# Optimization experiments

Hardware: AMD Instinct MI355X
Metric: run time of the kernel (lower is better)

Reference implementation:

```python
import jax, jax.numpy as jnp
import numpy as np

N, E = 4096, 131072
IN, HID, OUT = 128, 128, 256
H4, C4 = 4, HID            # first/middle GAT: 4 heads of 128 -> concat 512
CAT = H4 * C4              # 512
NH, DK = 8, OUT // 8       # dense MHA
EPS_LN = 1e-5


def setup_inputs() -> dict:
    key = jax.random.key(0)
    ks = jax.random.split(key, 32)
    s = 0.05
    inp = {
        "x": jax.random.normal(ks[0], (N, IN), jnp.float32),
        "edge_index": jax.random.randint(ks[1], (2, E), 0, N, jnp.int64),
        # GAT layer 0: in=128, heads=4, out=128
        "W0": jax.random.normal(ks[2], (IN, H4 * C4)) * s,
        "as0": jax.random.normal(ks[3], (H4, C4)) * s,
        "ad0": jax.random.normal(ks[4], (H4, C4)) * s,
        "b0": jnp.zeros((H4 * C4,)),
        # GAT layer 1: in=512, heads=4, out=128
        "W1": jax.random.normal(ks[5], (CAT, H4 * C4)) * s,
        "as1": jax.random.normal(ks[6], (H4, C4)) * s,
        "ad1": jax.random.normal(ks[7], (H4, C4)) * s,
        "b1": jnp.zeros((H4 * C4,)),
        # GAT layer 2: in=512, heads=1, out=256
        "W2": jax.random.normal(ks[8], (CAT, OUT)) * s,
        "as2": jax.random.normal(ks[9], (1, OUT)) * s,
        "ad2": jax.random.normal(ks[10], (1, OUT)) * s,
        "b2": jnp.zeros((OUT,)),
        # LayerNorms
        "g0": jnp.ones((CAT,)), "be0": jnp.zeros((CAT,)),
        "g1": jnp.ones((CAT,)), "be1": jnp.zeros((CAT,)),
        "g2": jnp.ones((OUT,)), "be2": jnp.zeros((OUT,)),
        # dense MHA on output_dim=256
        "wq": jax.random.normal(ks[11], (OUT, OUT)) * s, "bq": jnp.zeros((OUT,)),
        "wk": jax.random.normal(ks[12], (OUT, OUT)) * s, "bk": jnp.zeros((OUT,)),
        "wv": jax.random.normal(ks[13], (OUT, OUT)) * s, "bv": jnp.zeros((OUT,)),
        "wo": jax.random.normal(ks[14], (OUT, OUT)) * s, "bo": jnp.zeros((OUT,)),
    }
    return inp


def _layer_norm(x, g, b):
    mu = x.mean(-1, keepdims=True)
    var = ((x - mu) ** 2).mean(-1, keepdims=True)
    return (x - mu) * jax.lax.rsqrt(var + EPS_LN) * g + b


def _gat(x, src, dst, W, a_src, a_dst, bias, heads, out_c):
    # PyG GATConv (concat=True, negative_slope=0.2, self-loops pre-added)
    n = x.shape[0]
    xl = (x @ W).reshape(n, heads, out_c)            # [N,H,C]
    al_s = (xl * a_src).sum(-1)                      # [N,H]
    al_d = (xl * a_dst).sum(-1)                      # [N,H]
    alpha = jax.nn.leaky_relu(al_s[src] + al_d[dst], 0.2)  # [Etot,H]
    m = jax.ops.segment_max(alpha, dst, num_segments=n)
    e = jnp.exp(alpha - m[dst])
    denom = jax.ops.segment_sum(e, dst, num_segments=n)
    w = e / (denom[dst] + 1e-16)                     # [Etot,H]
    msg = w[:, :, None] * xl[src]                    # [Etot,H,C]
    out = jax.ops.segment_sum(msg, dst, num_segments=n)
    return out.reshape(n, heads * out_c) + bias


def _mha(x, wq, bq, wk, bk, wv, bv, wo, bo):
    # x: [1,N,D], 8 heads
    B, S, D = x.shape
    def split(y):
        return y.reshape(B, S, NH, DK).transpose(0, 2, 1, 3)
    Q, K, V = split(x @ wq + bq), split(x @ wk + bk), split(x @ wv + bv)
    scores = jnp.einsum('bhqd,bhkd->bhqk', Q, K) / np.sqrt(DK)
    attn = jax.nn.softmax(scores, axis=-1)
    out = jnp.einsum('bhqk,bhkd->bhqd', attn, V)
    out = out.transpose(0, 2, 1, 3).reshape(B, S, D)
    return out @ wo + bo


def reference(x, edge_index, W0, as0, ad0, b0, W1, as1, ad1, b1, W2, as2, ad2, b2,
              g0, be0, g1, be1, g2, be2, wq, bq, wk, bk, wv, bv, wo, bo):
    n = x.shape[0]
    loops = jnp.arange(n, dtype=edge_index.dtype)
    src = jnp.concatenate([edge_index[0], loops])
    dst = jnp.concatenate([edge_index[1], loops])

    # layer 0: in=128 -> 512; residual None (128 != 512)
    h = jax.nn.elu(_gat(x, src, dst, W0, as0, ad0, b0, H4, C4))
    h = _layer_norm(h, g0, be0)

    # layer 1: 512 -> 512; residual applies
    res = h
    h = jax.nn.elu(_gat(h, src, dst, W1, as1, ad1, b1, H4, C4))
    h = _layer_norm(h, g1, be1)
    h = h + res

    # layer 2: 512 -> 256, 1 head
    h = _gat(h, src, dst, W2, as2, ad2, b2, 1, OUT)
    h = _layer_norm(h, g2, be2)

    # dense self-attention over all nodes as one sequence
    h = _mha(h[None], wq, bq, wk, bk, wv, bv, wo, bo)[0]
    return h
```

## Files before the change

kernel.cpp:

```cpp
#include <hip/hip_runtime.h>
#include <math.h>

typedef __attribute__((ext_vector_type(8))) short short8;
typedef __attribute__((ext_vector_type(4))) float float4v;

#define QS 0.17677669529663687f

__device__ __forceinline__ float waveReduceSum(float v){
  #pragma unroll
  for(int o=32;o>0;o>>=1) v += __shfl_down(v,o,64);
  return v;
}

__device__ __forceinline__ unsigned short f2bf(float f){
  unsigned int u = __float_as_uint(f);
  return (unsigned short)((u + 0x7FFFu + ((u>>16)&1u)) >> 16);
}
__device__ __forceinline__ float bf2f(unsigned short u){
  return __uint_as_float(((unsigned int)u)<<16);
}

__global__ __launch_bounds__(256) void prep(const float* __restrict__ x, unsigned short* __restrict__ xb,
                     const float* __restrict__ W0, unsigned short* __restrict__ W0t,
                     const float* __restrict__ W1, unsigned short* __restrict__ W1t,
                     const float* __restrict__ W2, unsigned short* __restrict__ W2t,
                     const float* __restrict__ wq, const float* __restrict__ wk,
                     const float* __restrict__ wv, unsigned short* __restrict__ wqkvt,
                     const float* __restrict__ bq, const float* __restrict__ bk,
                     const float* __restrict__ bv, float* __restrict__ bqkv,
                     const float* __restrict__ wo, unsigned short* __restrict__ wot,
                     const float* __restrict__ as0, const float* __restrict__ ad0, unsigned short* __restrict__ S0,
                     const float* __restrict__ as1, const float* __restrict__ ad1, unsigned short* __restrict__ S1,
                     const float* __restrict__ as2, const float* __restrict__ ad2, unsigned short* __restrict__ S2){
  int b = blockIdx.x, t = threadIdx.x;
  if(b < 2048){ int i = b*256 + t; xb[i] = f2bf(x[i]); return; }
  if(b == 4864){ bqkv[t] = bq[t]*QS; bqkv[256+t] = bk[t]; bqkv[512+t] = bv[t]; return; }
  if(b >= 4865){
    int bb = b - 4865;
    const float *W,*as,*ad; unsigned short* S; int K,C,H,k;
    if(bb<128){W=W0;as=as0;ad=ad0;S=S0;K=128;C=128;H=4;k=bb;}
    else if(bb<640){W=W1;as=as1;ad=ad1;S=S1;K=512;C=128;H=4;k=bb-128;}
    else {W=W2;as=as2;ad=ad2;S=S2;K=512;C=256;H=1;k=bb-640;}
    int D = H*C;
    __shared__ float s1[4], s2[4];
    int lane=t&63, wid=t>>6;
    for(int h=0;h<H;h++){
      float ps=0.f, pd=0.f;
      for(int c=t;c<C;c+=256){
        float wv2 = W[k*D + h*C + c];
        ps += wv2*as[h*C+c];
        pd += wv2*ad[h*C+c];
      }
      ps = waveReduceSum(ps); pd = waveReduceSum(pd);
      if(lane==0){ s1[wid]=ps; s2[wid]=pd; }
      __syncthreads();
      if(t==0){
        float u=s1[0]+s1[1]+s1[2]+s1[3], v=s2[0]+s2[1]+s2[2]+s2[3];
        S[h*K+k]=f2bf(u); S[(4+h)*K+k]=f2bf(v);
      }
      __syncthreads();
    }
    if(t==0){
      for(int h=H;h<4;h++){ S[h*K+k]=0; S[(4+h)*K+k]=0; }
      for(int r=8;r<16;r++) S[r*K+k]=0;
    }
    return;
  }
  const float* src; unsigned short* dst; int K,N,base,roff; float sc = 1.f;
  if(b<2304){src=W0;dst=W0t;K=128;N=512;base=2048;roff=0;}
  else if(b<3328){src=W1;dst=W1t;K=512;N=512;base=2304;roff=0;}
  else if(b<3840){src=W2;dst=W2t;K=512;N=256;base=3328;roff=0;}
  else if(b<4096){src=wq;dst=wqkvt;K=256;N=256;base=3840;roff=0;sc=QS;}
  else if(b<4352){src=wk;dst=wqkvt;K=256;N=256;base=4096;roff=256;}
  else if(b<4608){src=wv;dst=wqkvt;K=256;N=256;base=4352;roff=512;}
  else            {src=wo;dst=wot;K=256;N=256;base=4608;roff=0;}
  int idx = (b-base)*256 + t;
  int k = idx / N, n = idx - k*N;
  dst[(n+roff)*K + k] = f2bf(src[idx]*sc);
}

__global__ __launch_bounds__(256) void gemm_mfma(const unsigned short* __restrict__ A,
                                                 const unsigned short* __restrict__ Bt,
                                                 const float* __restrict__ bias,
                                                 float* __restrict__ C,
                                                 unsigned short* __restrict__ Cb,
                                                 const unsigned short* __restrict__ Wsd,
                                                 float* __restrict__ als,
                                                 float* __restrict__ ald,
                                                 int M, int K, int N){
  int t = threadIdx.x, lane = t & 63, w = t >> 6;
  int m = lane & 15, g = lane >> 4;
  int bm = blockIdx.y * 64, bn = blockIdx.x * 64;

  __shared__ unsigned short As[64*72];
  __shared__ unsigned short Bs[64*72];

  int sr = t >> 3;
  int sc = (t & 7) * 8;
  const unsigned short* Ap = A  + (bm + sr)*K + sc;
  const unsigned short* Bp = Bt + (bn + sr)*K + sc;
  bool doC = (Wsd != nullptr) && (blockIdx.x == 0);

  float4v acc[4];
  #pragma unroll
  for(int nt=0;nt<4;nt++) acc[nt] = (float4v){0.f,0.f,0.f,0.f};
  float4v acc2 = (float4v){0.f,0.f,0.f,0.f};

  for(int k0=0;k0<K;k0+=64){
    short8 a0 = *(const short8*)(Ap + k0);
    short8 a1 = *(const short8*)(Ap + 32*K + k0);
    short8 b0 = *(const short8*)(Bp + k0);
    short8 b1 = *(const short8*)(Bp + 32*K + k0);
    __syncthreads();
    *(short8*)&As[sr*72 + sc]      = a0;
    *(short8*)&As[(sr+32)*72 + sc] = a1;
    *(short8*)&Bs[sr*72 + sc]      = b0;
    *(short8*)&Bs[(sr+32)*72 + sc] = b1;
    __syncthreads();

    #pragma unroll
    for(int ks=0;ks<2;ks++){
      short8 aA = *(const short8*)&As[(w*16 + m)*72 + ks*32 + g*8];
      #pragma unroll
      for(int nt=0;nt<4;nt++){
        short8 bB = *(const short8*)&Bs[(nt*16 + m)*72 + ks*32 + g*8];
        acc[nt] = __builtin_amdgcn_mfma_f32_16x16x32_bf16(aA, bB, acc[nt], 0,0,0);
      }
      if(doC){
        short8 bW = *(const short8*)(Wsd + m*K + k0 + ks*32 + g*8);
        acc2 = __builtin_amdgcn_mfma_f32_16x16x32_bf16(aA, bW, acc2, 0,0,0);
      }
    }
  }
  #pragma unroll
  for(int nt=0;nt<4;nt++){
    int col = bn + nt*16 + m;
    float bv = bias ? bias[col] : 0.f;
    #pragma unroll
    for(int r=0;r<4;r++){
      int row = bm + w*16 + g*4 + r;
      float v = acc[nt][r] + bv;
      if(C)  C[row*N + col]  = v;
      if(Cb) Cb[row*N + col] = f2bf(v);
    }
  }
  if(doC){
    #pragma unroll
    for(int r=0;r<4;r++){
      int row = bm + w*16 + g*4 + r;
      if(m<4)      als[row*4 + m]     = acc2[r];
      else if(m<8) ald[row*4 + (m-4)] = acc2[r];
    }
  }
}

__global__ void csr_count(const int* __restrict__ ei, int E, int Etot,
                          int* __restrict__ hist){
  int e = blockIdx.x*256 + threadIdx.x;
  if(e>=Etot) return;
  int d = (e<E) ? (ei[E+e]&4095) : (e-E);
  atomicAdd(&hist[d], 1);
}

__global__ __launch_bounds__(1024) void csr_scan(const int* __restrict__ hist,
                                                 int* __restrict__ row_ptr,
                                                 int* __restrict__ wcnt, int N){
  __shared__ int sh[1024];
  int t = threadIdx.x;
  int base[4];
  int s = 0;
  #pragma unroll
  for(int i=0;i<4;i++){ base[i]=s; s += hist[t*4+i]; }
  sh[t] = s;
  __syncthreads();
  for(int off=1; off<1024; off<<=1){
    int x = (t>=off) ? sh[t-off] : 0;
    __syncthreads();
    sh[t] += x;
    __syncthreads();
  }
  int excl = (t==0) ? 0 : sh[t-1];
  #pragma unroll
  for(int i=0;i<4;i++){
    row_ptr[t*4+i] = excl + base[i];
    wcnt[t*4+i]    = excl + base[i];
  }
  if(t==1023) row_ptr[N] = excl + s;
}

__global__ void csr_scatter(const int* __restrict__ ei, int E, int Etot,
                            int* __restrict__ wcnt, int* __restrict__ col){
  int e = blockIdx.x*256 + threadIdx.x;
  if(e>=Etot) return;
  int s,d;
  if(e<E){ s=ei[e]&4095; d=ei[E+e]&4095; } else { s=d=e-E; }
  int pos = atomicAdd(&wcnt[d], 1);
  col[pos] = s;
}

#define CE 128
__global__ void gat_gather_ln(const int* __restrict__ rp,
                              const int* __restrict__ col,
                              const unsigned short* __restrict__ xlb,
                              const float* __restrict__ als,
                              const float* __restrict__ ald,
                              const float* __restrict__ bias,
                              const float* __restrict__ gw,
                              const float* __restrict__ be,
                              const float* __restrict__ res,
                              float* __restrict__ out,
                              unsigned short* __restrict__ outb,
                              int D, int logC, int do_elu){
  int n = blockIdx.x, t = threadIdx.x;
  int c0 = t*2;
  int h = c0 >> logC;
  int rowW = D >> 1;
  float4 advv = *(const float4*)(ald + n*4);
  int start = rp[n], end = rp[n+1];
  const unsigned int* xw = (const unsigned int*)xlb;

  __shared__ float pw[CE*4];
  __shared__ int offs[CE];

  float acc0=0.f, acc1=0.f, den=0.f;

  for(int base=start; base<end; base+=CE){
    int cnt = min(CE, end-base);
    __syncthreads();
    if(t < cnt){
      int s = col[base+t];
      offs[t] = s*rowW;
      float4 av = *(const float4*)(als + s*4);
      #pragma unroll
      for(int hh=0;hh<4;hh++){
        float a = ((const float*)&av)[hh] + ((const float*)&advv)[hh];
        a = a>0.f ? a : 0.2f*a;
        pw[t*4+hh] = __expf(a);
      }
    }
    __syncthreads();
    #pragma unroll 4
    for(int j=0;j<cnt;j++){
      float p = pw[j*4+h];
      unsigned int u = xw[offs[j] + t];
      acc0 += p * bf2f((unsigned short)(u & 0xffffu));
      acc1 += p * bf2f((unsigned short)(u >> 16));
      den += p;
    }
  }

  float inv_d = 1.f/(den + 1e-16f);
  float v0 = acc0*inv_d + bias[c0];
  float v1 = acc1*inv_d + bias[c0+1];
  if(do_elu){
    v0 = v0>0.f ? v0 : expm1f(v0);
    v1 = v1>0.f ? v1 : expm1f(v1);
  }
  __shared__ float sh[4];
  int lane=t&63, wid=t>>6, nw = blockDim.x>>6;
  float sum = waveReduceSum(v0+v1);
  if(lane==0) sh[wid]=sum;
  __syncthreads();
  float mean = 0.f;
  for(int i=0;i<nw;i++) mean += sh[i];
  mean /= (float)D;
  __syncthreads();
  float d0 = v0-mean, d1 = v1-mean;
  float vs = waveReduceSum(d0*d0 + d1*d1);
  if(lane==0) sh[wid]=vs;
  __syncthreads();
  float var = 0.f;
  for(int i=0;i<nw;i++) var += sh[i];
  var /= (float)D;
  float inv = rsqrtf(var + 1e-5f);
  float y0 = d0*inv*gw[c0]   + be[c0];
  float y1 = d1*inv*gw[c0+1] + be[c0+1];
  if(res){ float2 rv = *(const float2*)(res + n*D + c0); y0 += rv.x; y1 += rv.y; }
  if(out) *(float2*)(out + n*D + c0) = make_float2(y0, y1);
  if(outb) ((unsigned int*)outb)[n*rowW + t] =
      (unsigned int)f2bf(y0) | ((unsigned int)f2bf(y1) << 16);
}

__global__ __launch_bounds__(256) void transpose_v(const unsigned short* __restrict__ QKV,
                                                   unsigned short* __restrict__ Vt, int S){
  __shared__ unsigned short tile[64][72];
  int bs = blockIdx.x*64;
  int bd = blockIdx.y*64;
  int t = threadIdx.x;
  int r8 = t>>3, c8 = (t&7)*8;
  #pragma unroll
  for(int it=0; it<2; it++){
    int row = r8 + it*32;
    short8 v = *(const short8*)(QKV + (bs+row)*768 + 512 + bd + c8);
    *(short8*)&tile[row][c8] = v;
  }
  __syncthreads();
  #pragma unroll
  for(int it=0; it<2; it++){
    int drow = r8 + it*32;
    short8 o;
    #pragma unroll
    for(int j=0;j<8;j++) o[j] = (short)tile[c8+j][drow];
    *(short8*)(Vt + (bd+drow)*S + bs + c8) = o;
  }
}

#define KS 4
__global__ __launch_bounds__(256) void attention10(const unsigned short* __restrict__ QKV,
                                                   const unsigned short* __restrict__ Vt,
                                                   float* __restrict__ Op,
                                                   float* __restrict__ lp, int S){
  const int RS = 768;
  int qb = blockIdx.x * 64;
  int h  = blockIdx.y;
  int ks = blockIdx.z;
  int t  = threadIdx.x;
  int lane = t & 63, w = t >> 6;
  int m = lane & 15, g = lane >> 4;

  __shared__ unsigned short Ps[64*72];
  __shared__ unsigned short Vs[32*72];
  __shared__ unsigned short Ks[64*36];

  short8 aQ = *(const short8*)(QKV + (qb + w*16 + m)*RS + h*32 + g*8);

  float4v o0 = {0.f,0.f,0.f,0.f}, o1 = {0.f,0.f,0.f,0.f};
  float l = 0.f;

  int r8 = t>>3, c8 = (t&7)*8;
  int kr = t>>2, kc = (t&3)*8;
  int kA = ks*(S/KS), kB = kA + S/KS;

  for(int kt=kA; kt<kB; kt+=64){
    short8 v = *(const short8*)(Vt + (h*32 + r8)*S + kt + c8);
    short8 kv = *(const short8*)(QKV + (kt + kr)*RS + 256 + h*32 + kc);
    __syncthreads();
    *(short8*)&Vs[r8*72 + c8] = v;
    *(short8*)&Ks[kr*36 + kc] = kv;
    __syncthreads();

    #pragma unroll
    for(int nt=0;nt<4;nt++){
      short8 aK = *(const short8*)&Ks[(nt*16 + m)*36 + g*8];
      float4v acc = {0.f,0.f,0.f,0.f};
      acc = __builtin_amdgcn_mfma_f32_16x16x32_bf16(aK, aQ, acc, 0,0,0);
      float p0 = __expf(acc[0]);
      float p1 = __expf(acc[1]);
      float p2 = __expf(acc[2]);
      float p3 = __expf(acc[3]);
      l += (p0+p1) + (p2+p3);
      unsigned int r0 = __float_as_uint(p0) + 0x8000u;
      unsigned int r1 = __float_as_uint(p1) + 0x8000u;
      unsigned int r2 = __float_as_uint(p2) + 0x8000u;
      unsigned int r3 = __float_as_uint(p3) + 0x8000u;
      uint2 pk;
      pk.x = __builtin_amdgcn_perm(r1, r0, 0x07060302u);
      pk.y = __builtin_amdgcn_perm(r3, r2, 0x07060302u);
      *(uint2*)&Ps[(w*16 + m)*72 + nt*16 + g*4] = pk;
    }

    #pragma unroll
    for(int kh=0;kh<2;kh++){
      short8 aP  = *(const short8*)&Ps[(w*16 + m)*72 + kh*32 + g*8];
      short8 bV0 = *(const short8*)&Vs[(m)*72    + kh*32 + g*8];
      short8 bV1 = *(const short8*)&Vs[(16+m)*72 + kh*32 + g*8];
      o0 = __builtin_amdgcn_mfma_f32_16x16x32_bf16(aP, bV0, o0, 0,0,0);
      o1 = __builtin_amdgcn_mfma_f32_16x16x32_bf16(aP, bV1, o1, 0,0,0);
    }
  }

  l += __shfl_xor(l, 16, 64);
  l += __shfl_xor(l, 32, 64);

  float* Ob = Op + (size_t)ks*S*256;
  #pragma unroll
  for(int r=0;r<4;r++){
    int q = qb + w*16 + g*4 + r;
    Ob[q*256 + h*32 + m]      = o0[r];
    Ob[q*256 + h*32 + 16 + m] = o1[r];
  }
  if(g==0) lp[ks*S*8 + (qb + w*16 + m)*8 + h] = l;
}

__global__ __launch_bounds__(256) void combine(const float* __restrict__ Op,
                                               const float* __restrict__ lp,
                                               unsigned short* __restrict__ aob, int S){
  int q = blockIdx.x, t = threadIdx.x;
  int h = t >> 5;
  float o = 0.f, l = 0.f;
  #pragma unroll
  for(int s=0;s<KS;s++) o += Op[(size_t)s*S*256 + q*256 + t];
  #pragma unroll
  for(int s=0;s<KS;s++) l += lp[s*S*8 + q*8 + h];
  aob[q*256 + t] = f2bf(o / l);
}

extern "C" void kernel_launch(void* const* d_in, const int* in_sizes, int n_in,
                              void* d_out, int out_size, void* d_ws, size_t ws_size,
                              hipStream_t stream) {
  const float* x   = (const float*)d_in[0];
  const int*   ei  = (const int*)d_in[1];
  const float* W0  = (const float*)d_in[2];
  const float* as0 = (const float*)d_in[3];
  const float* ad0 = (const float*)d_in[4];
  const float* b0  = (const float*)d_in[5];
  const float* W1  = (const float*)d_in[6];
  const float* as1 = (const float*)d_in[7];
  const float* ad1 = (const float*)d_in[8];
  const float* b1  = (const float*)d_in[9];
  const float* W2  = (const float*)d_in[10];
  const float* as2 = (const float*)d_in[11];
  const float* ad2 = (const float*)d_in[12];
  const float* b2  = (const float*)d_in[13];
  const float* g0  = (const float*)d_in[14];
  const float* be0 = (const float*)d_in[15];
  const float* g1  = (const float*)d_in[16];
  const float* be1 = (const float*)d_in[17];
  const float* g2  = (const float*)d_in[18];
  const float* be2 = (const float*)d_in[19];
  const float* wq  = (const float*)d_in[20];
  const float* bq  = (const float*)d_in[21];
  const float* wk  = (const float*)d_in[22];
  const float* bk  = (const float*)d_in[23];
  const float* wv  = (const float*)d_in[24];
  const float* bv  = (const float*)d_in[25];
  const float* wo  = (const float*)d_in[26];
  const float* bo  = (const float*)d_in[27];
  float* out = (float*)d_out;

  const int N = 4096;
  const int E = in_sizes[1] / 2;
  const int Etot = E + N;

  char* p = (char*)d_ws;
  auto alloc = [&](size_t bytes){ char* r = p; p += (bytes + 255) & ~(size_t)255; return r; };

  float* h0   = (float*)alloc(N*512*4);
  float* als  = (float*)alloc(N*4*4);
  float* ald  = (float*)alloc(N*4*4);
  unsigned short* xb   = (unsigned short*)alloc(N*128*2);
  unsigned short* xlb  = (unsigned short*)alloc(N*512*2);
  unsigned short* h0b  = (unsigned short*)alloc(N*512*2);
  unsigned short* h1b  = (unsigned short*)alloc(N*512*2);
  unsigned short* h2b  = (unsigned short*)alloc(N*256*2);
  unsigned short* QKVb = (unsigned short*)alloc((size_t)N*768*2);
  unsigned short* Vt   = (unsigned short*)alloc(256*N*2);
  unsigned short* aob  = (unsigned short*)alloc(N*256*2);
  unsigned short* W0t  = (unsigned short*)alloc(512*128*2);
  unsigned short* W1t  = (unsigned short*)alloc(512*512*2);
  unsigned short* W2t  = (unsigned short*)alloc(256*512*2);
  unsigned short* wqkvt= (unsigned short*)alloc(768*256*2);
  float* bqkv = (float*)alloc(768*4);
  unsigned short* wot  = (unsigned short*)alloc(256*256*2);
  unsigned short* Wsd0 = (unsigned short*)alloc(16*128*2);
  unsigned short* Wsd1 = (unsigned short*)alloc(16*512*2);
  unsigned short* Wsd2 = (unsigned short*)alloc(16*512*2);
  float* Op = (float*)alloc((size_t)KS*N*256*4);
  float* lp = (float*)alloc((size_t)KS*N*8*4);
  int* hist = (int*)alloc(N*4);
  int* wcnt = (int*)alloc(N*4);
  int* rp   = (int*)alloc((N+2)*4);
  int* col  = (int*)alloc(Etot*4);

  prep<<<6017, 256, 0, stream>>>(x, xb, W0, W0t, W1, W1t, W2, W2t,
                                 wq, wk, wv, wqkvt, bq, bk, bv, bqkv, wo, wot,
                                 as0, ad0, Wsd0, as1, ad1, Wsd1, as2, ad2, Wsd2);

  hipMemsetAsync(hist, 0, N*sizeof(int), stream);
  csr_count<<<(Etot+255)/256, 256, 0, stream>>>(ei, E, Etot, hist);
  csr_scan<<<1, 1024, 0, stream>>>(hist, rp, wcnt, N);
  csr_scatter<<<(Etot+255)/256, 256, 0, stream>>>(ei, E, Etot, wcnt, col);

  gemm_mfma<<<dim3(8, 64), 256, 0, stream>>>(xb, W0t, nullptr, nullptr, xlb, Wsd0, als, ald, N, 128, 512);
  gat_gather_ln<<<N, 256, 0, stream>>>(rp, col, xlb, als, ald, b0, g0, be0,
                                       nullptr, h0, h0b, 512, 7, 1);

  gemm_mfma<<<dim3(8, 64), 256, 0, stream>>>(h0b, W1t, nullptr, nullptr, xlb, Wsd1, als, ald, N, 512, 512);
  gat_gather_ln<<<N, 256, 0, stream>>>(rp, col, xlb, als, ald, b1, g1, be1,
                                       h0, nullptr, h1b, 512, 7, 1);

  gemm_mfma<<<dim3(4, 64), 256, 0, stream>>>(h1b, W2t, nullptr, nullptr, xlb, Wsd2, als, ald, N, 512, 256);
  gat_gather_ln<<<N, 128, 0, stream>>>(rp, col, xlb, als, ald, b2, g2, be2,
                                       nullptr, nullptr, h2b, 256, 8, 0);

  gemm_mfma<<<dim3(12, 64), 256, 0, stream>>>(h2b, wqkvt, bqkv, nullptr, QKVb, nullptr, nullptr, nullptr, N, 256, 768);
  transpose_v<<<dim3(N/64, 4), 256, 0, stream>>>(QKVb, Vt, N);
  attention10<<<dim3(N/64, 8, KS), 256, 0, stream>>>(QKVb, Vt, Op, lp, N);
  combine<<<N, 256, 0, stream>>>(Op, lp, aob, N);
  gemm_mfma<<<dim3(4, 64), 256, 0, stream>>>(aob, wot, bo, out, nullptr, nullptr, nullptr, nullptr, N, 256, 256);
}
```

Baseline: 286.6 us.

## Double-buffer GEMM LDS tiles and XOR-swizzle attention P/V shared memory

The GEMM kernel now uses two LDS buffers and prefetches the next K-tile into registers while the current tile is consumed, dropping one barrier per iteration. The intent is to hide global load latency behind MFMA work. The attention kernel replaces padded shared-memory rows (stride 72) with an XOR-swizzled 64-wide layout for the P and V tiles, aimed at avoiding LDS bank conflicts with less shared memory. In exchange, the GEMM doubles its LDS footprint, which may lower occupancy.

```diff
diff --git a/kernel.cpp b/kernel.cpp
--- a/kernel.cpp
+++ b/kernel.cpp
@@ -92,8 +92,8 @@
   int m = lane & 15, g = lane >> 4;
   int bm = blockIdx.y * 64, bn = blockIdx.x * 64;
 
-  __shared__ unsigned short As[64*72];
-  __shared__ unsigned short Bs[64*72];
+  __shared__ unsigned short As[2][64*72];
+  __shared__ unsigned short Bs[2][64*72];
 
   int sr = t >> 3;
   int sc = (t & 7) * 8;
@@ -106,24 +106,31 @@
   for(int nt=0;nt<4;nt++) acc[nt] = (float4v){0.f,0.f,0.f,0.f};
   float4v acc2 = (float4v){0.f,0.f,0.f,0.f};
 
+  short8 a0 = *(const short8*)(Ap);
+  short8 a1 = *(const short8*)(Ap + 32*K);
+  short8 b0 = *(const short8*)(Bp);
+  short8 b1 = *(const short8*)(Bp + 32*K);
+
+  int buf = 0;
   for(int k0=0;k0<K;k0+=64){
-    short8 a0 = *(const short8*)(Ap + k0);
-    short8 a1 = *(const short8*)(Ap + 32*K + k0);
-    short8 b0 = *(const short8*)(Bp + k0);
-    short8 b1 = *(const short8*)(Bp + 32*K + k0);
-    __syncthreads();
-    *(short8*)&As[sr*72 + sc]      = a0;
-    *(short8*)&As[(sr+32)*72 + sc] = a1;
-    *(short8*)&Bs[sr*72 + sc]      = b0;
-    *(short8*)&Bs[(sr+32)*72 + sc] = b1;
+    *(short8*)&As[buf][sr*72 + sc]      = a0;
+    *(short8*)&As[buf][(sr+32)*72 + sc] = a1;
+    *(short8*)&Bs[buf][sr*72 + sc]      = b0;
+    *(short8*)&Bs[buf][(sr+32)*72 + sc] = b1;
+    if(k0+64 < K){
+      a0 = *(const short8*)(Ap + k0+64);
+      a1 = *(const short8*)(Ap + 32*K + k0+64);
+      b0 = *(const short8*)(Bp + k0+64);
+      b1 = *(const short8*)(Bp + 32*K + k0+64);
+    }
     __syncthreads();
 
     #pragma unroll
     for(int ks=0;ks<2;ks++){
-      short8 aA = *(const short8*)&As[(w*16 + m)*72 + ks*32 + g*8];
+      short8 aA = *(const short8*)&As[buf][(w*16 + m)*72 + ks*32 + g*8];
       #pragma unroll
       for(int nt=0;nt<4;nt++){
-        short8 bB = *(const short8*)&Bs[(nt*16 + m)*72 + ks*32 + g*8];
+        short8 bB = *(const short8*)&Bs[buf][(nt*16 + m)*72 + ks*32 + g*8];
         acc[nt] = __builtin_amdgcn_mfma_f32_16x16x32_bf16(aA, bB, acc[nt], 0,0,0);
       }
       if(doC){
@@ -131,6 +138,7 @@
         acc2 = __builtin_amdgcn_mfma_f32_16x16x32_bf16(aA, bW, acc2, 0,0,0);
       }
     }
+    buf ^= 1;
   }
   #pragma unroll
   for(int nt=0;nt<4;nt++){
@@ -306,7 +314,7 @@
 }
 
 #define KS 4
-__global__ __launch_bounds__(256) void attention10(const unsigned short* __restrict__ QKV,
+__global__ __launch_bounds__(256) void attention11(const unsigned short* __restrict__ QKV,
                                                    const unsigned short* __restrict__ Vt,
                                                    float* __restrict__ Op,
                                                    float* __restrict__ lp, int S){
@@ -317,9 +325,10 @@
   int t  = threadIdx.x;
   int lane = t & 63, w = t >> 6;
   int m = lane & 15, g = lane >> 4;
-
-  __shared__ unsigned short Ps[64*72];
-  __shared__ unsigned short Vs[32*72];
+  int m7 = m & 7;
+
+  __shared__ unsigned short Ps[64*64];
+  __shared__ unsigned short Vs[32*64];
   __shared__ unsigned short Ks[64*36];
 
   short8 aQ = *(const short8*)(QKV + (qb + w*16 + m)*RS + h*32 + g*8);
@@ -327,15 +336,15 @@
   float4v o0 = {0.f,0.f,0.f,0.f}, o1 = {0.f,0.f,0.f,0.f};
   float l = 0.f;
 
-  int r8 = t>>3, c8 = (t&7)*8;
+  int r8 = t>>3, c8 = t&7;
   int kr = t>>2, kc = (t&3)*8;
   int kA = ks*(S/KS), kB = kA + S/KS;
 
   for(int kt=kA; kt<kB; kt+=64){
-    short8 v = *(const short8*)(Vt + (h*32 + r8)*S + kt + c8);
+    short8 v = *(const short8*)(Vt + (h*32 + r8)*S + kt + c8*8);
     short8 kv = *(const short8*)(QKV + (kt + kr)*RS + 256 + h*32 + kc);
     __syncthreads();
-    *(short8*)&Vs[r8*72 + c8] = v;
+    *(short8*)&Vs[r8*64 + ((c8 ^ (r8&7))<<3)] = v;
     *(short8*)&Ks[kr*36 + kc] = kv;
     __syncthreads();
 
@@ -356,14 +365,15 @@
       uint2 pk;
       pk.x = __builtin_amdgcn_perm(r1, r0, 0x07060302u);
       pk.y = __builtin_amdgcn_perm(r3, r2, 0x07060302u);
-      *(uint2*)&Ps[(w*16 + m)*72 + nt*16 + g*4] = pk;
+      *(uint2*)&Ps[(w*16 + m)*64 + (((2*nt + (g>>1)) ^ m7)<<3) + ((g&1)<<2)] = pk;
     }
 
     #pragma unroll
     for(int kh=0;kh<2;kh++){
-      short8 aP  = *(const short8*)&Ps[(w*16 + m)*72 + kh*32 + g*8];
-      short8 bV0 = *(const short8*)&Vs[(m)*72    + kh*32 + g*8];
-      short8 bV1 = *(const short8*)&Vs[(16+m)*72 + kh*32 + g*8];
+      int swz = ((kh*4 + g) ^ m7) << 3;
+      short8 aP  = *(const short8*)&Ps[(w*16 + m)*64 + swz];
+      short8 bV0 = *(const short8*)&Vs[m*64       + swz];
+      short8 bV1 = *(const short8*)&Vs[(16+m)*64  + swz];
       o0 = __builtin_amdgcn_mfma_f32_16x16x32_bf16(aP, bV0, o0, 0,0,0);
       o1 = __builtin_amdgcn_mfma_f32_16x16x32_bf16(aP, bV1, o1, 0,0,0);
     }
@@ -485,7 +495,7 @@
 
   gemm_mfma<<<dim3(12, 64), 256, 0, stream>>>(h2b, wqkvt, bqkv, nullptr, QKVb, nullptr, nullptr, nullptr, N, 256, 768);
   transpose_v<<<dim3(N/64, 4), 256, 0, stream>>>(QKVb, Vt, N);
-  attention10<<<dim3(N/64, 8, KS), 256, 0, stream>>>(QKVb, Vt, Op, lp, N);
+  attention11<<<dim3(N/64, 8, KS), 256, 0, stream>>>(QKVb, Vt, Op, lp, N);
   combine<<<N, 256, 0, stream>>>(Op, lp, aob, N);
   gemm_mfma<<<dim3(4, 64), 256, 0, stream>>>(aob, wot, bo, out, nullptr, nullptr, nullptr, nullptr, N, 256, 256);
 }
```

After: 284.4 us. About the same (-0.8%).
